# Optimization experiments

Hardware: AMD Instinct MI355X
Metric: run time of the kernel (lower is better)

## Reference

```python
import jax, jax.numpy as jnp
import numpy as np

N_NODES = 100000


def setup_inputs() -> dict:
    key = jax.random.key(0)
    ks = jax.random.split(key, 7)
    n, d, c, e = N_NODES, 256, 128, 3200000
    features = jax.random.normal(ks[0], (n, d), dtype=jnp.float32)
    adj_row = jax.random.randint(ks[1], (e,), 0, n, dtype=jnp.int32)
    adj_col = jax.random.randint(ks[2], (e,), 0, n, dtype=jnp.int32)
    adj_vals = jax.random.uniform(ks[3], (e,), dtype=jnp.float32)
    kernel = jax.random.normal(ks[4], (d, c), dtype=jnp.float32) * (1.0 / np.sqrt(d))
    bias = jax.random.normal(ks[5], (c,), dtype=jnp.float32) * 0.01
    skip_weight = jax.random.normal(ks[6], (c,), dtype=jnp.float32)
    return {"features": features, "adj_row": adj_row, "adj_col": adj_col,
            "adj_vals": adj_vals, "kernel": kernel, "bias": bias,
            "skip_weight": skip_weight}


def reference(features, adj_row, adj_col, adj_vals, kernel, bias, skip_weight):
    # h = X @ W  : [n, c]
    h = features @ kernel
    # SpMM: out[r] += A[r, c] * h[c] over edges (COO)
    msgs = adj_vals[:, None] * h[adj_col]            # [e, c]
    agg = jax.ops.segment_sum(msgs, adj_row, num_segments=N_NODES)  # [n, c]
    out = h * skip_weight + agg                      # skip-connection scale + aggregation
    out = out + bias
    return jax.nn.selu(out)
```

## Files before the change

kernel.cpp:

```cpp
#include <hip/hip_runtime.h>
#include <math.h>

#define N_NODES 100000
#define D 256
#define C 128
#define N_EDGES 3200000

#define BROWS 128
#define NBUCKET ((N_NODES + BROWS - 1) / BROWS)
#define CAP 4608
#define EPB 8192
#define PBLOCKS ((N_EDGES + EPB - 1) / EPB)

typedef __attribute__((ext_vector_type(8))) short bf16x8;
typedef __attribute__((ext_vector_type(4))) float f32x4;

__device__ __forceinline__ unsigned short f2bf(float f) {
  const unsigned int u = __float_as_uint(f);
  return (unsigned short)((u + 0x7fffu + ((u >> 16) & 1u)) >> 16);
}
__device__ __forceinline__ unsigned int pack_bf(float lo, float hi) {
  return (unsigned int)f2bf(lo) | ((unsigned int)f2bf(hi) << 16);
}
__device__ __forceinline__ float bflo(unsigned int u) {
  return __uint_as_float(u << 16);
}
__device__ __forceinline__ float bfhi(unsigned int u) {
  return __uint_as_float(u & 0xffff0000u);
}
__device__ __forceinline__ float selu1(float x) {
  const float scale = 1.0507009873554804934193349852946f;
  const float alpha = 1.6732632423543772848170429916717f;
  return x > 0.f ? scale * x : scale * alpha * (__expf(x) - 1.f);
}
__device__ __forceinline__ unsigned int pack_rec(int col, float val) {
  return ((unsigned int)col << 15) | ((unsigned int)f2bf(val) & 0x7fffu);
}
__device__ __forceinline__ float rec_val(unsigned int r) {
  return __uint_as_float((r & 0x7fffu) << 16);
}
__device__ __forceinline__ bf16x8 packA_nt(const float* p) {
  const f32x4 a0 = __builtin_nontemporal_load(reinterpret_cast<const f32x4*>(p));
  const f32x4 a1 =
      __builtin_nontemporal_load(reinterpret_cast<const f32x4*>(p) + 1);
  union {
    unsigned int u[4];
    bf16x8 v;
  } af;
  af.u[0] = pack_bf(a0[0], a0[1]);
  af.u[1] = pack_bf(a0[2], a0[3]);
  af.u[2] = pack_bf(a1[0], a1[1]);
  af.u[3] = pack_bf(a1[2], a1[3]);
  return af.v;
}

__global__ __launch_bounds__(256) void prep(const float* __restrict__ W,
                                            unsigned short* __restrict__ WT,
                                            int* __restrict__ gcur) {
  const int t = blockIdx.x * blockDim.x + threadIdx.x;
  const int n = t >> 8;
  const int k = t & 255;
  WT[t] = f2bf(W[k * C + n]);
  if (t < NBUCKET) gcur[t] = 0;
}

__global__ __launch_bounds__(512) void gemm_partition(
    const float* __restrict__ X, const unsigned short* __restrict__ WT,
    unsigned short* __restrict__ h2, const int* __restrict__ row,
    const int* __restrict__ col, const float* __restrict__ vals,
    int* __restrict__ gcur, uint2* __restrict__ recs) {
  __shared__ int hist[NBUCKET];
  __shared__ int sbase[NBUCKET];
  const int bid = blockIdx.x;
  const int tid = threadIdx.x;

  if ((bid & 1) == 0) {
    const int wid = (bid >> 1) * 8 + (tid >> 6);
    const int row0 = wid * 32;
    if (row0 >= N_NODES) return;
    const int lane = tid & 63;
    const int r = lane & 15;
    const int kg = lane >> 4;

    f32x4 acc[2][8];
#pragma unroll
    for (int g = 0; g < 2; ++g)
#pragma unroll
      for (int f = 0; f < 8; ++f) acc[g][f] = (f32x4){0.f, 0.f, 0.f, 0.f};

    const float* arow0 = X + (size_t)(row0 + r) * D + kg * 8;
    const float* arow1 = arow0 + 16 * D;
    for (int k0 = 0; k0 < D; k0 += 32) {
      const bf16x8 a0 = packA_nt(arow0 + k0);
      const bf16x8 a1 = packA_nt(arow1 + k0);
#pragma unroll
      for (int f = 0; f < 8; ++f) {
        const bf16x8 bf = *reinterpret_cast<const bf16x8*>(
            WT + (size_t)(f * 16 + r) * D + k0 + kg * 8);
        acc[0][f] =
            __builtin_amdgcn_mfma_f32_16x16x32_bf16(a0, bf, acc[0][f], 0, 0, 0);
        acc[1][f] =
            __builtin_amdgcn_mfma_f32_16x16x32_bf16(a1, bf, acc[1][f], 0, 0, 0);
      }
    }
#pragma unroll
    for (int g = 0; g < 2; ++g)
#pragma unroll
      for (int f = 0; f < 8; ++f)
#pragma unroll
        for (int j = 0; j < 4; ++j)
          h2[(size_t)(row0 + g * 16 + kg * 4 + j) * C + f * 16 + r] =
              f2bf(acc[g][f][j]);
  } else {
    const int pb = bid >> 1;
    const int e0 = pb * EPB;
    for (int i = tid; i < NBUCKET; i += 512) hist[i] = 0;
    __syncthreads();

    unsigned int stash[16];
#pragma unroll
    for (int k = 0; k < 16; ++k) {
      const int e = e0 + k * 512 + tid;
      unsigned int s = 0xFFFFFFFFu;
      if (e < N_EDGES) {
        const int r = __builtin_nontemporal_load(row + e);
        const int off = atomicAdd(&hist[r >> 7], 1);
        s = (unsigned int)r | ((unsigned int)off << 17);
      }
      stash[k] = s;
    }
    __syncthreads();
    for (int b = tid; b < NBUCKET; b += 512) {
      const int h = hist[b];
      sbase[b] = h ? atomicAdd(&gcur[b], h) : 0;
    }
    __syncthreads();
#pragma unroll
    for (int k = 0; k < 16; ++k) {
      const unsigned int s = stash[k];
      if (s == 0xFFFFFFFFu) continue;
      const int r = (int)(s & 0x1FFFFu);
      const int off = (int)(s >> 17);
      const int e = e0 + k * 512 + tid;
      const int c = __builtin_nontemporal_load(col + e);
      const float v = __builtin_nontemporal_load(vals + e);
      const int b = r >> 7;
      const int pos = sbase[b] + off;
      if (pos < CAP)
        recs[(size_t)b * CAP + pos] =
            make_uint2(pack_rec(c, v), r & (BROWS - 1));
    }
  }
}

__global__ __launch_bounds__(512) void sort_gather_selu(
    const int* __restrict__ gcur, const uint2* __restrict__ recs,
    const unsigned int* __restrict__ h2u, const float* __restrict__ skip,
    const float* __restrict__ bias, float* __restrict__ out) {
  __shared__ unsigned int sorted[CAP];
  __shared__ int hist[BROWS];
  __shared__ int start[BROWS];
  const int tid = threadIdx.x;
  const int b = blockIdx.x;

  int fill = gcur[b];
  fill = fill < CAP ? fill : CAP;

  if (tid < BROWS) hist[tid] = 0;
  __syncthreads();

  uint2 stash[9];
  int nst = 0;
  const unsigned long long* rb64 =
      reinterpret_cast<const unsigned long long*>(recs + (size_t)b * CAP);
  for (int i = tid; i < fill; i += 512) {
    const unsigned long long rc = __builtin_nontemporal_load(rb64 + i);
    const unsigned int cv = (unsigned int)rc;
    const unsigned int lr = (unsigned int)(rc >> 32);
    const int off = atomicAdd(&hist[lr], 1);
    stash[nst] = make_uint2(cv, lr | ((unsigned int)off << 7));
    ++nst;
  }
  __syncthreads();

  if (tid < BROWS) start[tid] = hist[tid];
  __syncthreads();
  for (int off = 1; off < BROWS; off <<= 1) {
    int t = 0;
    if (tid < BROWS && tid >= off) t = start[tid - off];
    __syncthreads();
    if (tid < BROWS) start[tid] += t;
    __syncthreads();
  }

  for (int k = 0; k < nst; ++k) {
    const int lr = (int)(stash[k].y & 127u);
    const int off = (int)(stash[k].y >> 7);
    sorted[start[lr] - hist[lr] + off] = stash[k].x;
  }
  __syncthreads();

  const int lane = tid & 63;
  const int wv = tid >> 6;
  for (int lr = wv; lr < BROWS; lr += 8) {
    const int grow = b * BROWS + lr;
    if (grow >= N_NODES) break;
    const int je = start[lr];
    int j = je - hist[lr];
    float ax = 0.f, ay = 0.f;
    for (; j + 7 < je; j += 8) {
      unsigned int cc[8], uu[8];
#pragma unroll
      for (int q = 0; q < 8; ++q) cc[q] = sorted[j + q];
#pragma unroll
      for (int q = 0; q < 8; ++q)
        uu[q] = h2u[(size_t)(cc[q] >> 15) * 64 + lane];
#pragma unroll
      for (int q = 0; q < 8; ++q) {
        ax = fmaf(rec_val(cc[q]), bflo(uu[q]), ax);
        ay = fmaf(rec_val(cc[q]), bfhi(uu[q]), ay);
      }
    }
    for (; j + 3 < je; j += 4) {
      unsigned int cc[4], uu[4];
#pragma unroll
      for (int q = 0; q < 4; ++q) cc[q] = sorted[j + q];
#pragma unroll
      for (int q = 0; q < 4; ++q)
        uu[q] = h2u[(size_t)(cc[q] >> 15) * 64 + lane];
#pragma unroll
      for (int q = 0; q < 4; ++q) {
        ax = fmaf(rec_val(cc[q]), bflo(uu[q]), ax);
        ay = fmaf(rec_val(cc[q]), bfhi(uu[q]), ay);
      }
    }
    for (; j < je; ++j) {
      const unsigned int cc = sorted[j];
      const unsigned int u = h2u[(size_t)(cc >> 15) * 64 + lane];
      ax = fmaf(rec_val(cc), bflo(u), ax);
      ay = fmaf(rec_val(cc), bfhi(u), ay);
    }
    const unsigned int hr = h2u[(size_t)grow * 64 + lane];
    const float2 sk = *reinterpret_cast<const float2*>(skip + lane * 2);
    const float2 bi = *reinterpret_cast<const float2*>(bias + lane * 2);
    const float ox = selu1(fmaf(bflo(hr), sk.x, ax) + bi.x);
    const float oy = selu1(fmaf(bfhi(hr), sk.y, ay) + bi.y);
    *reinterpret_cast<float2*>(out + (size_t)grow * C + lane * 2) =
        make_float2(ox, oy);
  }
}

extern "C" void kernel_launch(void* const* d_in, const int* in_sizes, int n_in,
                              void* d_out, int out_size, void* d_ws,
                              size_t ws_size, hipStream_t stream) {
  const float* features = (const float*)d_in[0];
  const int* adj_row = (const int*)d_in[1];
  const int* adj_col = (const int*)d_in[2];
  const float* adj_vals = (const float*)d_in[3];
  const float* W = (const float*)d_in[4];
  const float* bias = (const float*)d_in[5];
  const float* skip = (const float*)d_in[6];
  float* out = (float*)d_out;

  char* ws = (char*)d_ws;
  const size_t SZ_H2 = (size_t)N_NODES * C * 2;
  const size_t OFF_RECS = (SZ_H2 + 255) & ~(size_t)255;
  const size_t SZ_RECS = (size_t)NBUCKET * CAP * 8;
  const size_t OFF_GCUR = OFF_RECS + SZ_RECS;
  const size_t SZ_GCUR = (size_t)NBUCKET * 4;
  const size_t OFF_WT = (OFF_GCUR + SZ_GCUR + 255) & ~(size_t)255;
  const size_t NEEDED = OFF_WT + (size_t)D * C * 2;

  if (ws_size < NEEDED) return;

  unsigned short* h2 = (unsigned short*)ws;
  uint2* recs = (uint2*)(ws + OFF_RECS);
  int* gcur = (int*)(ws + OFF_GCUR);
  unsigned short* WT = (unsigned short*)(ws + OFF_WT);

  prep<<<(D * C) / 256, 256, 0, stream>>>(W, WT, gcur);

  gemm_partition<<<2 * PBLOCKS, 512, 0, stream>>>(
      features, WT, h2, adj_row, adj_col, adj_vals, gcur, recs);

  sort_gather_selu<<<NBUCKET, 512, 0, stream>>>(
      gcur, recs, (const unsigned int*)h2, skip, bias, out);
}
```

Measured before the change: 283.9 us.

## Replace global atomic bucket cursors with per-block local partitions and metadata scan

The partition step no longer reserves slots in global per-bucket arrays with atomics. Each partition block now does a local exclusive scan over its bucket histogram, writes its records contiguously into its own EPB-sized slab, and stores a packed (offset, count) entry per bucket in a metadata table. The consumer kernel reads the 391 metadata entries for its bucket, prefix-scans them, and locates each record's source segment with a binary search. This removes global atomic contention and the gcur reset, at the cost of scattered segment reads, an extra scan in both kernels, and a binary search for every loaded record.

```diff
diff --git a/kernel.cpp b/kernel.cpp
--- a/kernel.cpp
+++ b/kernel.cpp
@@ -55,22 +55,21 @@
 }
 
 __global__ __launch_bounds__(256) void prep(const float* __restrict__ W,
-                                            unsigned short* __restrict__ WT,
-                                            int* __restrict__ gcur) {
+                                            unsigned short* __restrict__ WT) {
   const int t = blockIdx.x * blockDim.x + threadIdx.x;
   const int n = t >> 8;
   const int k = t & 255;
   WT[t] = f2bf(W[k * C + n]);
-  if (t < NBUCKET) gcur[t] = 0;
 }
 
 __global__ __launch_bounds__(512) void gemm_partition(
     const float* __restrict__ X, const unsigned short* __restrict__ WT,
     unsigned short* __restrict__ h2, const int* __restrict__ row,
     const int* __restrict__ col, const float* __restrict__ vals,
-    int* __restrict__ gcur, uint2* __restrict__ recs) {
+    unsigned int* __restrict__ meta, uint2* __restrict__ recs) {
   __shared__ int hist[NBUCKET];
-  __shared__ int sbase[NBUCKET];
+  __shared__ int scanA[1024];
+  __shared__ int scanB[1024];
   const int bid = blockIdx.x;
   const int tid = threadIdx.x;
 
@@ -130,11 +129,27 @@
       stash[k] = s;
     }
     __syncthreads();
+
+    for (int i = tid; i < 1024; i += 512) scanA[i] = (i < NBUCKET) ? hist[i] : 0;
+    __syncthreads();
+    int* src = scanA;
+    int* dst = scanB;
+    for (int off = 1; off < 1024; off <<= 1) {
+      for (int i = tid; i < 1024; i += 512)
+        dst[i] = src[i] + ((i >= off) ? src[i - off] : 0);
+      __syncthreads();
+      int* tp = src;
+      src = dst;
+      dst = tp;
+    }
     for (int b = tid; b < NBUCKET; b += 512) {
-      const int h = hist[b];
-      sbase[b] = h ? atomicAdd(&gcur[b], h) : 0;
-    }
-    __syncthreads();
+      const int sb = src[b] - hist[b];
+      dst[b] = sb;
+      meta[(size_t)pb * NBUCKET + b] =
+          ((unsigned int)sb << 16) | (unsigned int)hist[b];
+    }
+    __syncthreads();
+
 #pragma unroll
     for (int k = 0; k < 16; ++k) {
       const unsigned int s = stash[k];
@@ -145,36 +160,60 @@
       const int c = __builtin_nontemporal_load(col + e);
       const float v = __builtin_nontemporal_load(vals + e);
       const int b = r >> 7;
-      const int pos = sbase[b] + off;
-      if (pos < CAP)
-        recs[(size_t)b * CAP + pos] =
-            make_uint2(pack_rec(c, v), r & (BROWS - 1));
+      recs[(size_t)pb * EPB + dst[b] + off] =
+          make_uint2(pack_rec(c, v), r & (BROWS - 1));
     }
   }
 }
 
 __global__ __launch_bounds__(512) void sort_gather_selu(
-    const int* __restrict__ gcur, const uint2* __restrict__ recs,
+    const unsigned int* __restrict__ meta, const uint2* __restrict__ recs,
     const unsigned int* __restrict__ h2u, const float* __restrict__ skip,
     const float* __restrict__ bias, float* __restrict__ out) {
   __shared__ unsigned int sorted[CAP];
   __shared__ int hist[BROWS];
   __shared__ int start[BROWS];
+  __shared__ int segA[512];
+  __shared__ int segB[512];
+  __shared__ unsigned int segglob[PBLOCKS];
   const int tid = threadIdx.x;
   const int b = blockIdx.x;
 
-  int fill = gcur[b];
-  fill = fill < CAP ? fill : CAP;
+  int cnt = 0;
+  if (tid < PBLOCKS) {
+    const unsigned int m = meta[(size_t)tid * NBUCKET + b];
+    cnt = (int)(m & 0xFFFFu);
+    segglob[tid] = (unsigned int)tid * EPB + (m >> 16);
+  }
+  segA[tid] = cnt;
+  __syncthreads();
+  int* s1 = segA;
+  int* s2 = segB;
+  for (int off = 1; off < 512; off <<= 1) {
+    s2[tid] = s1[tid] + ((tid >= off) ? s1[tid - off] : 0);
+    __syncthreads();
+    int* tp = s1;
+    s1 = s2;
+    s2 = tp;
+  }
+  const int fill0 = s1[PBLOCKS - 1];
+  const int fill = fill0 < CAP ? fill0 : CAP;
 
   if (tid < BROWS) hist[tid] = 0;
   __syncthreads();
 
   uint2 stash[9];
   int nst = 0;
-  const unsigned long long* rb64 =
-      reinterpret_cast<const unsigned long long*>(recs + (size_t)b * CAP);
   for (int i = tid; i < fill; i += 512) {
-    const unsigned long long rc = __builtin_nontemporal_load(rb64 + i);
+    int lo = 0, hi = PBLOCKS - 1;
+    while (lo < hi) {
+      const int mid = (lo + hi) >> 1;
+      if (s1[mid] > i) hi = mid;
+      else lo = mid + 1;
+    }
+    const int idx = i - (lo ? s1[lo - 1] : 0);
+    const unsigned long long rc = __builtin_nontemporal_load(
+        reinterpret_cast<const unsigned long long*>(recs) + segglob[lo] + idx);
     const unsigned int cv = (unsigned int)rc;
     const unsigned int lr = (unsigned int)(rc >> 32);
     const int off = atomicAdd(&hist[lr], 1);
@@ -213,8 +252,7 @@
 #pragma unroll
       for (int q = 0; q < 8; ++q) cc[q] = sorted[j + q];
 #pragma unroll
-      for (int q = 0; q < 8; ++q)
-        uu[q] = h2u[(size_t)(cc[q] >> 15) * 64 + lane];
+      for (int q = 0; q < 8; ++q) uu[q] = h2u[(size_t)(cc[q] >> 15) * 64 + lane];
 #pragma unroll
       for (int q = 0; q < 8; ++q) {
         ax = fmaf(rec_val(cc[q]), bflo(uu[q]), ax);
@@ -226,8 +264,7 @@
 #pragma unroll
       for (int q = 0; q < 4; ++q) cc[q] = sorted[j + q];
 #pragma unroll
-      for (int q = 0; q < 4; ++q)
-        uu[q] = h2u[(size_t)(cc[q] >> 15) * 64 + lane];
+      for (int q = 0; q < 4; ++q) uu[q] = h2u[(size_t)(cc[q] >> 15) * 64 + lane];
 #pragma unroll
       for (int q = 0; q < 4; ++q) {
         ax = fmaf(rec_val(cc[q]), bflo(uu[q]), ax);
@@ -265,24 +302,24 @@
   char* ws = (char*)d_ws;
   const size_t SZ_H2 = (size_t)N_NODES * C * 2;
   const size_t OFF_RECS = (SZ_H2 + 255) & ~(size_t)255;
-  const size_t SZ_RECS = (size_t)NBUCKET * CAP * 8;
-  const size_t OFF_GCUR = OFF_RECS + SZ_RECS;
-  const size_t SZ_GCUR = (size_t)NBUCKET * 4;
-  const size_t OFF_WT = (OFF_GCUR + SZ_GCUR + 255) & ~(size_t)255;
+  const size_t SZ_RECS = (size_t)PBLOCKS * EPB * 8;
+  const size_t OFF_META = OFF_RECS + SZ_RECS;
+  const size_t SZ_META = (size_t)PBLOCKS * NBUCKET * 4;
+  const size_t OFF_WT = (OFF_META + SZ_META + 255) & ~(size_t)255;
   const size_t NEEDED = OFF_WT + (size_t)D * C * 2;
 
   if (ws_size < NEEDED) return;
 
   unsigned short* h2 = (unsigned short*)ws;
   uint2* recs = (uint2*)(ws + OFF_RECS);
-  int* gcur = (int*)(ws + OFF_GCUR);
+  unsigned int* meta = (unsigned int*)(ws + OFF_META);
   unsigned short* WT = (unsigned short*)(ws + OFF_WT);
 
-  prep<<<(D * C) / 256, 256, 0, stream>>>(W, WT, gcur);
+  prep<<<(D * C) / 256, 256, 0, stream>>>(W, WT);
 
   gemm_partition<<<2 * PBLOCKS, 512, 0, stream>>>(
-      features, WT, h2, adj_row, adj_col, adj_vals, gcur, recs);
+      features, WT, h2, adj_row, adj_col, adj_vals, meta, recs);
 
   sort_gather_selu<<<NBUCKET, 512, 0, stream>>>(
-      gcur, recs, (const unsigned int*)h2, skip, bias, out);
-}
+      meta, recs, (const unsigned int*)h2, skip, bias, out);
+}
```

Measured after the change: 285.3 us. About the same (+0.5%).
